# Performance work log

Hardware: AMD Instinct MI355X
Metric: run time of the kernel (lower is better)

Reference implementation:

```python
import jax, jax.numpy as jnp
import numpy as np

B, C, H, W = 8, 512, 64, 64
WS, NH = 8, 16
HD = C // NH
SCALE = float(HD) ** -0.5
L = WS * WS  # tokens per window
BN_EPS = 1e-5


def _rel_index():
    # Swin relative position index, (L, L) int table into (2*WS-1)^2 bias rows
    ch = np.arange(WS)
    coords = np.stack(np.meshgrid(ch, ch, indexing='ij'))  # (2, WS, WS)
    cf = coords.reshape(2, -1)
    rel = cf[:, :, None] - cf[:, None, :]
    rel = rel.transpose(1, 2, 0).copy()
    rel[:, :, 0] += WS - 1
    rel[:, :, 1] += WS - 1
    rel[:, :, 0] *= 2 * WS - 1
    return jnp.asarray(rel.sum(-1))

REL_IDX = _rel_index()


def conv2d(x, w, pad=0, groups=1):
    return jax.lax.conv_general_dilated(
        x, w, (1, 1), [(pad, pad), (pad, pad)],
        feature_group_count=groups,
        dimension_numbers=('NCHW', 'OIHW', 'NCHW'))


def bn(x, g, b):
    # eval-mode BatchNorm with running_mean=0, running_var=1 (fresh init)
    inv = 1.0 / np.sqrt(1.0 + BN_EPS)
    return g[None, :, None, None] * (x * inv) + b[None, :, None, None]


def avgpool(x, kh, kw, ph, pw):
    # torch AvgPool2d: zero padding, count_include_pad=True
    s = jax.lax.reduce_window(x, 0.0, jax.lax.add, (1, 1, kh, kw), (1, 1, 1, 1),
                              ((0, 0), (0, 0), (ph, ph), (pw, pw)))
    return s / (kh * kw)


def setup_inputs() -> dict:
    key = jax.random.key(0)
    ks = jax.random.split(key, 8)
    r = lambda k, s: jax.random.normal(k, s, dtype=jnp.float32) * 0.02
    return {
        'x': jax.random.normal(ks[0], (B, C, H, W), dtype=jnp.float32),
        'w_lc1': r(ks[1], (C, C, 1, 1)),
        'g1': jnp.ones((C,), jnp.float32), 'b1': jnp.zeros((C,), jnp.float32),
        'w_lc2': r(ks[2], (C, C, 3, 3)),
        'g2': jnp.ones((C,), jnp.float32), 'b2': jnp.zeros((C,), jnp.float32),
        'w_qkv': r(ks[3], (3 * C, C, 1, 1)),
        'rel_table': r(ks[4], ((2 * WS - 1) * (2 * WS - 1), NH)),
        'w_dw': r(ks[5], (C, 1, WS, WS)),
        'g3': jnp.ones((C,), jnp.float32), 'b3': jnp.zeros((C,), jnp.float32),
        'w_pw': r(ks[6], (C, C, 1, 1)),
    }


def reference(x, w_lc1, g1, b1, w_lc2, g2, b2, w_qkv, rel_table, w_dw, g3, b3, w_pw):
    # local branch: 1x1 conv+BN  +  3x3 conv+BN
    local = bn(conv2d(x, w_lc1), g1, b1) + bn(conv2d(x, w_lc2, pad=1), g2, b2)

    # H, W divisible by WS -> pad() is a no-op; Hp, Wp = H, W
    hh, ww = H // WS, W // WS
    qkv = conv2d(x, w_qkv)  # (B, 3C, H, W)
    # 'b (qkv h d) (hh ws1) (ww ws2) -> qkv (b hh ww) h (ws1 ws2) d'
    qkv = qkv.reshape(B, 3, NH, HD, hh, WS, ww, WS)
    qkv = qkv.transpose(1, 0, 4, 6, 2, 5, 7, 3).reshape(3, B * hh * ww, NH, L, HD)
    q, k, v = qkv[0], qkv[1], qkv[2]

    dots = jnp.einsum('bhid,bhjd->bhij', q, k) * SCALE  # (Bw, NH, L, L)
    bias = rel_table[REL_IDX]                            # (L, L, NH)
    dots = dots + bias.transpose(2, 0, 1)[None]
    attn = jax.nn.softmax(dots, axis=-1)
    out = jnp.einsum('bhij,bhjd->bhid', attn, v)         # (Bw, NH, L, HD)

    # '(b hh ww) h (ws1 ws2) d -> b (h d) (hh ws1) (ww ws2)'
    out = out.reshape(B, hh, ww, NH, WS, WS, HD)
    out = out.transpose(0, 3, 6, 1, 4, 2, 5).reshape(B, C, H, W)

    ax = avgpool(jnp.pad(out, ((0, 0), (0, 0), (0, 1), (0, 0)), mode='reflect'),
                 WS, 1, WS // 2 - 1, 0)
    ay = avgpool(jnp.pad(out, ((0, 0), (0, 0), (0, 0), (0, 1)), mode='reflect'),
                 1, WS, 0, WS // 2 - 1)
    out = ax + ay + local

    # pad_out + SeparableConvBN(kernel=WS): depthwise conv -> BN -> 1x1 conv
    out = jnp.pad(out, ((0, 0), (0, 0), (0, 1), (0, 1)), mode='reflect')
    out = conv2d(out, w_dw, pad=(WS - 1) // 2, groups=C)
    out = bn(out, g3, b3)
    out = conv2d(out, w_pw)
    return out[:, :, :H, :W]
```

## Files before the change

### kernel.cpp

```cpp
#include <hip/hip_runtime.h>

#define INVBN 0.9999950000374997f
#define ATT_SCALE 0.17677669529663687f

typedef short bf16x8 __attribute__((ext_vector_type(8)));
typedef float f32x4  __attribute__((ext_vector_type(4)));
typedef unsigned short us8v __attribute__((ext_vector_type(8)));

#define AS1C(p) ((const __attribute__((address_space(1))) void*)(p))
#define AS3(p)  ((__attribute__((address_space(3))) void*)(p))

#define VMCNT_BARRIER(Nstr) do {                                   \
    asm volatile("s_waitcnt vmcnt(" Nstr ")" ::: "memory");        \
    __builtin_amdgcn_s_barrier(); } while (0)

__device__ __forceinline__ float bf2f(unsigned short u) {
    return __uint_as_float(((unsigned)u) << 16);
}
__device__ __forceinline__ unsigned short f2bf(float f) {
    unsigned u = __float_as_uint(f);
    u += 0x7FFFu + ((u >> 16) & 1u);
    return (unsigned short)(u >> 16);
}

__global__ __launch_bounds__(256)
void repack_kernel(const float* __restrict__ W2, const float* __restrict__ W1,
                   const float* __restrict__ Wq, const float* __restrict__ Wp,
                   const float* __restrict__ g1, const float* __restrict__ g2,
                   const float* __restrict__ b1, const float* __restrict__ b2,
                   unsigned short* __restrict__ Wt, unsigned short* __restrict__ WqO,
                   unsigned short* __restrict__ WpO, float* __restrict__ bsum)
{
    int i = blockIdx.x * 256 + threadIdx.x;
    if (i < 512) bsum[i] = b1[i] + b2[i];
    if (i < 786432) WqO[i] = f2bf(Wq[i]);
    if (i < 262144) WpO[i] = f2bf(Wp[i]);
    if (i >= 2359296) return;
    int tap = i / 262144;
    int rem = i - tap * 262144;
    int m   = rem >> 9;
    float v = g2[m] * INVBN * W2[(size_t)rem * 9 + tap];
    if (tap == 4) v = fmaf(g1[m] * INVBN, W1[rem], v);
    Wt[i] = f2bf(v);
}

__global__ __launch_bounds__(256)
void bias_precompute_kernel(const float* __restrict__ RT, float* __restrict__ biasM)
{
    int idx = blockIdx.x * 256 + threadIdx.x;
    int h = idx >> 10, rem = idx & 1023;
    int frag = rem >> 6, lane = rem & 63;
    int fi = frag >> 2, fj = frag & 3;
    int q  = 16 * fj + (lane & 15);
    int kb = 16 * fi + ((lane >> 4) << 2);
    int yi = q >> 3, xi = q & 7;
    float4 o;
    float* op = (float*)&o;
#pragma unroll
    for (int r = 0; r < 4; ++r) {
        int j = kb + r;
        int ridx = (yi - (j >> 3) + 7) * 15 + (xi - (j & 7) + 7);
        op[r] = RT[ridx * 16 + h];
    }
    *(float4*)&biasM[(size_t)idx * 4] = o;
}

__global__ __launch_bounds__(256)
void pad_transpose_kernel(const float* __restrict__ X, unsigned short* __restrict__ XT)
{
    int ph = blockIdx.x;
    int b  = blockIdx.y;
    int t  = threadIdx.x;
    unsigned short* rowbase = XT + ((size_t)b * 4356 + (size_t)ph * 66) * 512;
    uint4 z = make_uint4(0, 0, 0, 0);
    if (ph == 0 || ph == 65) {
        uint4* p4 = (uint4*)rowbase;
        for (int i = t; i < 4224; i += 256) p4[i] = z;
        return;
    }
    if (t < 64)       ((uint4*)rowbase)[t] = z;
    else if (t < 128) ((uint4*)(rowbase + 65 * 512))[t - 64] = z;

    int h = ph - 1;
    __shared__ float tile[64][65];
    const float* xb = X + (size_t)b * 512 * 4096 + h * 64;
    for (int cc = 0; cc < 8; ++cc) {
        int c0 = cc * 64;
        __syncthreads();
#pragma unroll
        for (int i = 0; i < 4; ++i) {
            int cl = i * 16 + (t >> 4);
            int w0 = (t & 15) * 4;
            *(float4*)&tile[cl][w0] =
                *(const float4*)&xb[(size_t)(c0 + cl) * 4096 + w0];
        }
        __syncthreads();
#pragma unroll
        for (int it = 0; it < 2; ++it) {
            int wl = it * 32 + (t >> 3);
            int cs = (t & 7) * 8;
            us8v v;
#pragma unroll
            for (int e = 0; e < 8; ++e) v[e] = f2bf(tile[cs + e][wl]);
            *(us8v*)&rowbase[(size_t)(1 + wl) * 512 + c0 + cs] = v;
        }
    }
}

template<int NTAPS>
__global__ __launch_bounds__(512, 2)
void mfma_gemm256(const unsigned short* __restrict__ A,
                  const unsigned short* __restrict__ Bw,
                  const float* __restrict__ bias,
                  unsigned short* __restrict__ Out, int M)
{
    __shared__ __align__(16) unsigned short ldsbuf[65536];

    const int t    = threadIdx.x;
    const int wid  = t >> 6, lane = t & 63;
    const int wr   = wid >> 2, wc = wid & 3;
    const int lrow = lane & 15, lk = lane >> 4;
    const int n0 = blockIdx.x * 256;
    const int m0 = blockIdx.y * 256;
    const int b  = blockIdx.z;
    const unsigned short* Ab = A + (size_t)b * (4356 * 512);
    unsigned short* Ob = Out + (size_t)b * ((size_t)M * 4096);

    const unsigned short* src[4];
    {
        int rsub = lane >> 2, ch = lane & 3;
        int chs  = ch ^ ((rsub >> 1) & 3);
#pragma unroll
        for (int i = 0; i < 4; ++i) {
            if (wid < 4) {
                int p = n0 + (wid * 4 + i) * 16 + rsub;
                int h = p >> 6, w = p & 63;
                src[i] = Ab + (size_t)((h + 1) * 66 + (w + 1)) * 512 + chs * 8;
            } else {
                int m = m0 + ((wid - 4) * 4 + i) * 16 + rsub;
                src[i] = Bw + (size_t)m * 512 + chs * 8;
            }
        }
    }

    f32x4 acc[8][4] = {};

    const int ck0 = (lk ^ ((lrow >> 1) & 3)) * 8;

    auto aScal = [&](int tt) -> int {
        if (NTAPS == 1) return tt * 32;
        int tap = tt >> 4;
        return (tap / 3 - 1) * (66 * 512) + (tap % 3 - 1) * 512 + (tt & 15) * 32;
    };
    auto bScal = [&](int tt) -> int {
        if (NTAPS == 1) return tt * 32;
        return (tt >> 4) * (M * 512) + (tt & 15) * 32;
    };
    auto STAGE = [&](int bufk, int aoff, int boff) {
        int off = (wid < 4) ? aoff : boff;
#pragma unroll
        for (int i = 0; i < 4; ++i)
            __builtin_amdgcn_global_load_lds(
                AS1C(src[i] + off),
                AS3(&ldsbuf[bufk * 16384 + (wid * 4 + i) * 512]), 16, 0, 0);
    };
    auto COMPUTE = [&](int bufk) {
        const unsigned short* Ak = &ldsbuf[bufk * 16384];
        const unsigned short* Bk = &ldsbuf[bufk * 16384 + 8192];
        bf16x8 af[8], bfr[4];
#pragma unroll
        for (int f = 0; f < 8; ++f)
            af[f] = *(const bf16x8*)&Ak[(wr * 128 + f * 16 + lrow) * 32 + ck0];
#pragma unroll
        for (int g = 0; g < 4; ++g)
            bfr[g] = *(const bf16x8*)&Bk[(wc * 64 + g * 16 + lrow) * 32 + ck0];
        __builtin_amdgcn_s_setprio(1);
#pragma unroll
        for (int f = 0; f < 8; ++f)
#pragma unroll
            for (int g = 0; g < 4; ++g)
                acc[f][g] = __builtin_amdgcn_mfma_f32_16x16x32_bf16(
                    af[f], bfr[g], acc[f][g], 0, 0, 0);
        __builtin_amdgcn_s_setprio(0);
    };

    constexpr int NT = NTAPS * 16;

    STAGE(0, aScal(0), bScal(0));
    STAGE(1, aScal(1), bScal(1));
    STAGE(2, aScal(2), bScal(2));
    VMCNT_BARRIER("8");

#pragma unroll 1
    for (int tb = 0; tb < NT - 4; tb += 4) {
        STAGE(3, aScal(tb + 3), bScal(tb + 3)); COMPUTE(0); VMCNT_BARRIER("8");
        STAGE(0, aScal(tb + 4), bScal(tb + 4)); COMPUTE(1); VMCNT_BARRIER("8");
        STAGE(1, aScal(tb + 5), bScal(tb + 5)); COMPUTE(2); VMCNT_BARRIER("8");
        STAGE(2, aScal(tb + 6), bScal(tb + 6)); COMPUTE(3); VMCNT_BARRIER("8");
    }
    STAGE(3, aScal(NT - 1), bScal(NT - 1)); COMPUTE(0); VMCNT_BARRIER("8");
    COMPUTE(1); VMCNT_BARRIER("4");
    COMPUTE(2); VMCNT_BARRIER("0");
    COMPUTE(3);

#pragma unroll
    for (int g = 0; g < 4; ++g) {
        int m = m0 + wc * 64 + g * 16 + lrow;
        float bv = bias ? bias[m] : 0.f;
        size_t mrow = (size_t)m * 4096;
#pragma unroll
        for (int f = 0; f < 8; ++f) {
            int nb = n0 + wr * 128 + f * 16 + lk * 4;
            f32x4 a4 = acc[f][g];
            ushort4 o;
            o.x = f2bf(a4[0] + bv);
            o.y = f2bf(a4[1] + bv);
            o.z = f2bf(a4[2] + bv);
            o.w = f2bf(a4[3] + bv);
            *(ushort4*)&Ob[mrow + nb] = o;
        }
    }
}

__global__ __launch_bounds__(256)
void mfma_gemm_f32out(const unsigned short* __restrict__ A,
                      const unsigned short* __restrict__ Bw,
                      float* __restrict__ Out, int M)
{
    __shared__ short As[128 * 64];
    __shared__ short Bs[128 * 64];

    const int t  = threadIdx.x;
    const int n0 = blockIdx.x * 128;
    const int m0 = blockIdx.y * 128;
    const int b  = blockIdx.z;
    const unsigned short* Ab = A + (size_t)b * (4096 * 512);
    float* Ob = Out + (size_t)b * ((size_t)M * 4096);

    const int trow = t >> 3;
    const int csrc = (t & 7) ^ (trow & 7);
    const unsigned short* aSrc[4];
    const unsigned short* bSrc[4];
#pragma unroll
    for (int i = 0; i < 4; ++i) {
        int r = i * 32 + trow;
        aSrc[i] = Ab + ((size_t)(n0 + r) * 512 + csrc * 8);
        bSrc[i] = Bw + ((size_t)(m0 + r) * 512 + csrc * 8);
    }
    short* aDst = As + (t & 192) * 8;
    short* bDst = Bs + (t & 192) * 8;

    const int lane = t & 63;
    const int wv = t >> 6, wr = wv >> 1, wc = wv & 1;
    const int lrow = lane & 15, lk = lane >> 4;
    int aOff[4][2], bOff[4][2];
#pragma unroll
    for (int f = 0; f < 4; ++f)
#pragma unroll
        for (int kk = 0; kk < 2; ++kk) {
            int ra = wr * 64 + f * 16 + lrow;
            aOff[f][kk] = ra * 64 + ((kk * 4 + lk) ^ (ra & 7)) * 8;
            int rb = wc * 64 + f * 16 + lrow;
            bOff[f][kk] = rb * 64 + ((kk * 4 + lk) ^ (rb & 7)) * 8;
        }

    f32x4 acc[4][4] = {};

#pragma unroll 1
    for (int ks = 0; ks < 8; ++ks) {
        const int k0 = ks * 64;
        __syncthreads();
#pragma unroll
        for (int i = 0; i < 4; ++i) {
            __builtin_amdgcn_global_load_lds(
                AS1C(aSrc[i] + k0), AS3(aDst + i * 2048), 16, 0, 0);
            __builtin_amdgcn_global_load_lds(
                AS1C(bSrc[i] + k0), AS3(bDst + i * 2048), 16, 0, 0);
        }
        __syncthreads();
        bf16x8 av[4][2], bv[4][2];
#pragma unroll
        for (int f = 0; f < 4; ++f) {
            av[f][0] = *(const bf16x8*)&As[aOff[f][0]];
            av[f][1] = *(const bf16x8*)&As[aOff[f][1]];
            bv[f][0] = *(const bf16x8*)&Bs[bOff[f][0]];
            bv[f][1] = *(const bf16x8*)&Bs[bOff[f][1]];
        }
#pragma unroll
        for (int kk = 0; kk < 2; ++kk)
#pragma unroll
            for (int fn = 0; fn < 4; ++fn)
#pragma unroll
                for (int fm = 0; fm < 4; ++fm)
                    acc[fn][fm] = __builtin_amdgcn_mfma_f32_16x16x32_bf16(
                        av[fn][kk], bv[fm][kk], acc[fn][fm], 0, 0, 0);
    }

#pragma unroll
    for (int fm = 0; fm < 4; ++fm) {
        int m = m0 + wc * 64 + fm * 16 + lrow;
        size_t mrow = (size_t)m * 4096;
#pragma unroll
        for (int fn = 0; fn < 4; ++fn) {
            int nb = n0 + wr * 64 + fn * 16 + lk * 4;
            f32x4 a4 = acc[fn][fm];
            *(float4*)&Ob[mrow + nb] = make_float4(a4[0], a4[1], a4[2], a4[3]);
        }
    }
}

__global__ __launch_bounds__(256)
void attn_mfma_kernel(const unsigned short* __restrict__ QKV,
                      const float* __restrict__ biasM,
                      float* __restrict__ OutB)
{
    __shared__ short smem[4 * 9216];
    int t = threadIdx.x;
    int wv = t >> 6, lane = t & 63;
    int wing = blockIdx.x >> 2;
    int head = (blockIdx.x & 3) * 4 + wv;
    int b    = blockIdx.y;
    int hhi = wing >> 3, wwi = wing & 7;
    int sp0 = hhi * 512 + wwi * 8;
    int ch0 = head * 32;
    const unsigned short* Qg = QKV + (size_t)b * 1536 * 4096;

    short* Qtm = smem + wv * 9216;
    short* Ktm = Qtm + 2304;
    short* Pq  = Qtm + 4608;

    {
        int d  = lane & 31;
        int rb = lane >> 5;
#pragma unroll
        for (int i = 0; i < 4; ++i) {
            int r = rb + 2 * i;
            us8v q8 = *(const us8v*)&Qg[(size_t)(ch0 + d) * 4096 + sp0 + r * 64];
            us8v k8 = *(const us8v*)&Qg[(size_t)(512 + ch0 + d) * 4096 + sp0 + r * 64];
#pragma unroll
            for (int e = 0; e < 8; ++e) {
                Qtm[(r * 8 + e) * 36 + d] = (short)q8[e];
                Ktm[(r * 8 + e) * 36 + d] = (short)k8[e];
            }
        }
    }

    int lrow = lane & 15, lk = lane >> 4;

    bf16x8 kf[4], qf[4];
#pragma unroll
    for (int f = 0; f < 4; ++f) {
        kf[f] = *(const bf16x8*)&Ktm[(lrow + 16 * f) * 36 + lk * 8];
        qf[f] = *(const bf16x8*)&Qtm[(lrow + 16 * f) * 36 + lk * 8];
    }
    f32x4 s[4][4] = {};
#pragma unroll
    for (int fi = 0; fi < 4; ++fi)
#pragma unroll
        for (int fj = 0; fj < 4; ++fj)
            s[fi][fj] = __builtin_amdgcn_mfma_f32_16x16x32_bf16(
                kf[fi], qf[fj], s[fi][fj], 0, 0, 0);

    const float* bM = biasM + (size_t)head * 4096;
    float rs[4];
#pragma unroll
    for (int fj = 0; fj < 4; ++fj) {
        float v[4][4];
#pragma unroll
        for (int fi = 0; fi < 4; ++fi) {
            float4 bv = *(const float4*)&bM[((fi * 4 + fj) * 64 + lane) * 4];
            const float* bvp = (const float*)&bv;
#pragma unroll
            for (int r = 0; r < 4; ++r)
                v[fi][r] = fmaf(s[fi][fj][r], ATT_SCALE, bvp[r]);
        }
        float m = -1e30f;
#pragma unroll
        for (int fi = 0; fi < 4; ++fi)
#pragma unroll
            for (int r = 0; r < 4; ++r) m = fmaxf(m, v[fi][r]);
        m = fmaxf(m, __shfl_xor(m, 16));
        m = fmaxf(m, __shfl_xor(m, 32));
        float ev[4][4];
        float sum = 0.f;
#pragma unroll
        for (int fi = 0; fi < 4; ++fi)
#pragma unroll
            for (int r = 0; r < 4; ++r) {
                ev[fi][r] = __expf(v[fi][r] - m);
                sum += ev[fi][r];
            }
        sum += __shfl_xor(sum, 16);
        sum += __shfl_xor(sum, 32);
        rs[fj] = 1.f / sum;
#pragma unroll
        for (int fi = 0; fi < 4; ++fi) {
            unsigned p0 = (unsigned)f2bf(ev[fi][0]) | ((unsigned)f2bf(ev[fi][1]) << 16);
            unsigned p1 = (unsigned)f2bf(ev[fi][2]) | ((unsigned)f2bf(ev[fi][3]) << 16);
            *(uint2*)&Pq[(lrow + 16 * fj) * 72 + 16 * fi + lk * 4] = make_uint2(p0, p1);
        }
    }

    f32x4 o[2][4] = {};
#pragma unroll
    for (int ks = 0; ks < 2; ++ks) {
        bf16x8 vf[2], pf[4];
#pragma unroll
        for (int fid = 0; fid < 2; ++fid)
            vf[fid] = *(const bf16x8*)&Qg[(size_t)(1024 + ch0 + 16 * fid + lrow) * 4096
                                          + sp0 + (lk + 4 * ks) * 64];
#pragma unroll
        for (int fjq = 0; fjq < 4; ++fjq)
            pf[fjq] = *(const bf16x8*)&Pq[(lrow + 16 * fjq) * 72 + ks * 32 + lk * 8];
#pragma unroll
        for (int fid = 0; fid < 2; ++fid)
#pragma unroll
            for (int fjq = 0; fjq < 4; ++fjq)
                o[fid][fjq] = __builtin_amdgcn_mfma_f32_16x16x32_bf16(
                    vf[fid], pf[fjq], o[fid][fjq], 0, 0, 0);
    }

    float* Out = OutB + (size_t)b * 512 * 4096;
#pragma unroll
    for (int fjq = 0; fjq < 4; ++fjq) {
        int q  = lrow + 16 * fjq;
        int sp = sp0 + ((q >> 3) << 6) + (q & 7);
        float rr = rs[fjq];
#pragma unroll
        for (int fid = 0; fid < 2; ++fid)
#pragma unroll
            for (int r = 0; r < 4; ++r) {
                int dch = 16 * fid + lk * 4 + r;
                Out[(size_t)(ch0 + dch) * 4096 + sp] = o[fid][fjq][r] * rr;
            }
    }
}

__global__ __launch_bounds__(256)
void pooldw_kernel(const float* __restrict__ A, const unsigned short* __restrict__ L,
                   const float* __restrict__ Wd,
                   const float* __restrict__ g3, const float* __restrict__ b3,
                   unsigned short* __restrict__ U)
{
    int bc = blockIdx.x;
    int c  = bc & 511;
    __shared__ float pad[72][72];
    int t = threadIdx.x;
    float* pf = &pad[0][0];
#pragma unroll
    for (int i = 0; i < 21; ++i) {
        int e = i * 256 + t;
        if (e < 5184) pf[e] = 0.f;
    }
    __syncthreads();

    const float* ap = A + (size_t)bc * 4096;
#pragma unroll
    for (int i = 0; i < 4; ++i) {
        int idx = i * 256 + t;
        int y = idx >> 4, x4 = (idx & 15) * 4;
        *(float4*)&pad[3 + y][4 + x4] = ((const float4*)ap)[idx];
    }
    if (t < 64)       pad[67][4 + t] = ap[62 * 64 + t];
    else if (t < 128) { int y = t - 64; pad[3 + y][68] = ap[y * 64 + 62]; }
    else if (t == 128) pad[67][68] = ap[62 * 64 + 62];
    __syncthreads();

    const unsigned short* lp = L + (size_t)bc * 4096;
    int u  = t & 15, rr = t >> 4;
    int w0 = u * 4;
    float4 res[4];
#pragma unroll
    for (int g = 0; g < 4; ++g) {
        int h = g * 16 + rr;
        float4 sx = make_float4(0.f, 0.f, 0.f, 0.f);
#pragma unroll
        for (int i = 0; i < 8; ++i) {
            float4 v = *(const float4*)&pad[h + i][4 + w0];
            sx.x += v.x; sx.y += v.y; sx.z += v.z; sx.w += v.w;
        }
        float win[12];
        *(float4*)&win[0] = *(const float4*)&pad[3 + h][w0];
        *(float4*)&win[4] = *(const float4*)&pad[3 + h][w0 + 4];
        *(float4*)&win[8] = *(const float4*)&pad[3 + h][w0 + 8];
        float4 sy = make_float4(0.f, 0.f, 0.f, 0.f);
#pragma unroll
        for (int i = 0; i < 8; ++i) {
            sy.x += win[1 + i];
            sy.y += win[2 + i];
            sy.z += win[3 + i];
            sy.w += win[4 + i];
        }
        ushort4 l4 = *(const ushort4*)&lp[h * 64 + w0];
        res[g].x = fmaf(0.125f, sx.x + sy.x, bf2f(l4.x));
        res[g].y = fmaf(0.125f, sx.y + sy.y, bf2f(l4.y));
        res[g].z = fmaf(0.125f, sx.z + sy.z, bf2f(l4.z));
        res[g].w = fmaf(0.125f, sx.w + sy.w, bf2f(l4.w));
    }
    __syncthreads();

#pragma unroll
    for (int g = 0; g < 4; ++g) {
        int h = g * 16 + rr;
        *(float4*)&pad[3 + h][4 + w0] = res[g];
    }
    __syncthreads();
    if (t < 64)       pad[67][4 + t] = pad[65][4 + t];
    else if (t < 128) { int y = t - 64; pad[3 + y][68] = pad[3 + y][66]; }
    else if (t == 128) pad[67][68] = pad[65][66];
    __syncthreads();

    const float* wdp = Wd + c * 64;
    float gc  = g3[c] * INVBN;
    float bcv = b3[c];
#pragma unroll
    for (int g = 0; g < 4; ++g) {
        int h = g * 16 + rr;
        float a0 = 0.f, a1 = 0.f, a2 = 0.f, a3 = 0.f;
#pragma unroll
        for (int i = 0; i < 8; ++i) {
            float win[12];
            *(float4*)&win[0] = *(const float4*)&pad[h + i][w0];
            *(float4*)&win[4] = *(const float4*)&pad[h + i][w0 + 4];
            *(float4*)&win[8] = *(const float4*)&pad[h + i][w0 + 8];
#pragma unroll
            for (int j = 0; j < 8; ++j) {
                float wv = wdp[i * 8 + j];
                a0 = fmaf(wv, win[1 + j], a0);
                a1 = fmaf(wv, win[2 + j], a1);
                a2 = fmaf(wv, win[3 + j], a2);
                a3 = fmaf(wv, win[4 + j], a3);
            }
        }
        ushort4 o;
        o.x = f2bf(gc * a0 + bcv);
        o.y = f2bf(gc * a1 + bcv);
        o.z = f2bf(gc * a2 + bcv);
        o.w = f2bf(gc * a3 + bcv);
        *(ushort4*)&U[(size_t)bc * 4096 + h * 64 + w0] = o;
    }
}

__global__ __launch_bounds__(256)
void transpose_cp_kernel(const unsigned short* __restrict__ U, unsigned short* __restrict__ Ut)
{
    int pt = blockIdx.x;
    int b  = blockIdx.y;
    const unsigned short* Ub = U + (size_t)b * 512 * 4096;
    unsigned short* Utb = Ut + (size_t)b * 4096 * 512;
    __shared__ unsigned short tile[64][72];
    int t = threadIdx.x;
    int p0 = pt * 64;

    for (int cc = 0; cc < 8; ++cc) {
        int c0 = cc * 64;
        __syncthreads();
        {
            int cl = t >> 2, px = (t & 3) * 16;
            const unsigned short* src = &Ub[(size_t)(c0 + cl) * 4096 + p0 + px];
            *(us8v*)&tile[cl][px]     = *(const us8v*)src;
            *(us8v*)&tile[cl][px + 8] = *(const us8v*)(src + 8);
        }
        __syncthreads();
        {
            int pl = t >> 2, cx = (t & 3) * 16;
            us8v o0, o1;
#pragma unroll
            for (int e = 0; e < 8; ++e) {
                o0[e] = tile[cx + e][pl];
                o1[e] = tile[cx + 8 + e][pl];
            }
            unsigned short* dst = &Utb[(size_t)(p0 + pl) * 512 + c0 + cx];
            *(us8v*)dst       = o0;
            *(us8v*)(dst + 8) = o1;
        }
    }
}

extern "C" void kernel_launch(void* const* d_in, const int* in_sizes, int n_in,
                              void* d_out, int out_size, void* d_ws, size_t ws_size,
                              hipStream_t stream)
{
    (void)in_sizes; (void)n_in; (void)out_size;
    const float* x     = (const float*)d_in[0];
    const float* w_lc1 = (const float*)d_in[1];
    const float* g1    = (const float*)d_in[2];
    const float* b1    = (const float*)d_in[3];
    const float* w_lc2 = (const float*)d_in[4];
    const float* g2    = (const float*)d_in[5];
    const float* b2    = (const float*)d_in[6];
    const float* w_qkv = (const float*)d_in[7];
    const float* rt    = (const float*)d_in[8];
    const float* w_dw  = (const float*)d_in[9];
    const float* g3    = (const float*)d_in[10];
    const float* b3    = (const float*)d_in[11];
    const float* w_pw  = (const float*)d_in[12];
    float* out = (float*)d_out;

    unsigned short* S        = (unsigned short*)d_ws;
    unsigned short* local_us = S;
    unsigned short* xt_us    = S + 16777216;
    unsigned short* u_us     = xt_us;
    unsigned short* wt3_us   = S + 34619392;
    unsigned short* wq_us    = S + 36978688;
    unsigned short* wpw_us   = S + 37765120;
    float*          bsum     = (float*)(S + 38027264);
    float*          biasM    = (float*)(S + 38028288);
    unsigned short* qkv_us   = S + 38552576;
    unsigned short* ut_us    = local_us;

    const bool full = ws_size >= (size_t)(38552576 + 50331648) * 2;

    repack_kernel<<<dim3(9216), 256, 0, stream>>>(w_lc2, w_lc1, w_qkv, w_pw,
                                                  g1, g2, b1, b2,
                                                  wt3_us, wq_us, wpw_us, bsum);
    bias_precompute_kernel<<<dim3(64), 256, 0, stream>>>(rt, biasM);
    pad_transpose_kernel<<<dim3(66, 8), 256, 0, stream>>>(x, xt_us);
    mfma_gemm256<9><<<dim3(16, 2, 8), 512, 0, stream>>>(
        xt_us, wt3_us, bsum, local_us, 512);

    if (full) {
        mfma_gemm256<1><<<dim3(16, 6, 8), 512, 0, stream>>>(
            xt_us, wq_us, nullptr, qkv_us, 1536);
        attn_mfma_kernel<<<dim3(256, 8), 256, 0, stream>>>(qkv_us, biasM, out);
    } else {
        for (int b = 0; b < 8; ++b) {
            mfma_gemm256<1><<<dim3(16, 6, 1), 512, 0, stream>>>(
                xt_us + (size_t)b * 4356 * 512, wq_us, nullptr, qkv_us, 1536);
            attn_mfma_kernel<<<dim3(256, 1), 256, 0, stream>>>(
                qkv_us, biasM, out + (size_t)b * 2097152);
        }
    }

    pooldw_kernel<<<dim3(4096), 256, 0, stream>>>(out, local_us, w_dw, g3, b3, u_us);
    transpose_cp_kernel<<<dim3(64, 8), 256, 0, stream>>>(u_us, ut_us);
    mfma_gemm_f32out<<<dim3(32, 4, 8), 256, 0, stream>>>(
        ut_us, wpw_us, out, 512);
}
```

Before: 473.9 us.

## Split GEMM k-step into interleaved halves and store attention output as bf16

The 256x256 MFMA GEMM main loop is restructured so each k-tile runs as two half-steps. Each half issues half of the next stage's global-to-LDS loads, with barriers between the LDS fragment reads and the MFMA bursts, so loads, LDS traffic and matrix math overlap more finely. Separately, the attention kernel now writes its output as bf16 into a workspace buffer aliased with the input-transpose region instead of fp32 into the final output, and the pool/depthwise kernel reads bf16. This halves the attention write and read traffic, at the cost of extra barriers per tile and reduced precision of the intermediate.

```diff
diff --git a/kernel.cpp b/kernel.cpp
--- a/kernel.cpp
+++ b/kernel.cpp
@@ -9,10 +9,6 @@
 
 #define AS1C(p) ((const __attribute__((address_space(1))) void*)(p))
 #define AS3(p)  ((__attribute__((address_space(3))) void*)(p))
-
-#define VMCNT_BARRIER(Nstr) do {                                   \
-    asm volatile("s_waitcnt vmcnt(" Nstr ")" ::: "memory");        \
-    __builtin_amdgcn_s_barrier(); } while (0)
 
 __device__ __forceinline__ float bf2f(unsigned short u) {
     return __uint_as_float(((unsigned)u) << 16);
@@ -107,6 +103,41 @@
     }
 }
 
+#define MF(A,B,C) __builtin_amdgcn_mfma_f32_16x16x32_bf16((A),(B),(C),0,0,0)
+
+#define TILE(BUF, SBUF, SAO, SBO, DOSTAGE, DOVM, VMSTR) do {                  \
+    bf16x8 aa[4], bb[4];                                                      \
+    _Pragma("unroll")                                                         \
+    for (int f = 0; f < 4; ++f) {                                             \
+        aa[f] = *(const bf16x8*)&ldsbuf[(BUF)*16384 + (wr*128 + f*16 + lrow)*32 + ck0]; \
+        bb[f] = *(const bf16x8*)&ldsbuf[(BUF)*16384 + 8192 + (wc*64 + f*16 + lrow)*32 + ck0]; \
+    }                                                                         \
+    if (DOSTAGE) STAGEH((SBUF), (SAO), (SBO), 0);                             \
+    __builtin_amdgcn_s_barrier();                                             \
+    __builtin_amdgcn_s_setprio(1);                                            \
+    _Pragma("unroll")                                                         \
+    for (int f = 0; f < 4; ++f)                                               \
+        _Pragma("unroll")                                                     \
+        for (int g = 0; g < 4; ++g)                                           \
+            acc[f][g] = MF(aa[f], bb[g], acc[f][g]);                          \
+    __builtin_amdgcn_s_setprio(0);                                            \
+    __builtin_amdgcn_s_barrier();                                             \
+    _Pragma("unroll")                                                         \
+    for (int f = 0; f < 4; ++f)                                               \
+        aa[f] = *(const bf16x8*)&ldsbuf[(BUF)*16384 + (wr*128 + (f+4)*16 + lrow)*32 + ck0]; \
+    if (DOSTAGE) STAGEH((SBUF), (SAO), (SBO), 1);                             \
+    if (DOVM) { asm volatile("s_waitcnt vmcnt(" VMSTR ")" ::: "memory"); }    \
+    __builtin_amdgcn_s_barrier();                                             \
+    __builtin_amdgcn_s_setprio(1);                                            \
+    _Pragma("unroll")                                                         \
+    for (int f = 0; f < 4; ++f)                                               \
+        _Pragma("unroll")                                                     \
+        for (int g = 0; g < 4; ++g)                                           \
+            acc[f+4][g] = MF(aa[f], bb[g], acc[f+4][g]);                      \
+    __builtin_amdgcn_s_setprio(0);                                            \
+    __builtin_amdgcn_s_barrier();                                             \
+} while (0)
+
 template<int NTAPS>
 __global__ __launch_bounds__(512, 2)
 void mfma_gemm256(const unsigned short* __restrict__ A,
@@ -144,7 +175,6 @@
     }
 
     f32x4 acc[8][4] = {};
-
     const int ck0 = (lk ^ ((lrow >> 1) & 3)) * 8;
 
     auto aScal = [&](int tt) -> int {
@@ -156,52 +186,34 @@
         if (NTAPS == 1) return tt * 32;
         return (tt >> 4) * (M * 512) + (tt & 15) * 32;
     };
-    auto STAGE = [&](int bufk, int aoff, int boff) {
+    auto STAGEH = [&](int bufk, int aoff, int boff, int half) {
         int off = (wid < 4) ? aoff : boff;
 #pragma unroll
-        for (int i = 0; i < 4; ++i)
+        for (int i = 2 * half; i < 2 * half + 2; ++i)
             __builtin_amdgcn_global_load_lds(
                 AS1C(src[i] + off),
                 AS3(&ldsbuf[bufk * 16384 + (wid * 4 + i) * 512]), 16, 0, 0);
     };
-    auto COMPUTE = [&](int bufk) {
-        const unsigned short* Ak = &ldsbuf[bufk * 16384];
-        const unsigned short* Bk = &ldsbuf[bufk * 16384 + 8192];
-        bf16x8 af[8], bfr[4];
-#pragma unroll
-        for (int f = 0; f < 8; ++f)
-            af[f] = *(const bf16x8*)&Ak[(wr * 128 + f * 16 + lrow) * 32 + ck0];
-#pragma unroll
-        for (int g = 0; g < 4; ++g)
-            bfr[g] = *(const bf16x8*)&Bk[(wc * 64 + g * 16 + lrow) * 32 + ck0];
-        __builtin_amdgcn_s_setprio(1);
-#pragma unroll
-        for (int f = 0; f < 8; ++f)
-#pragma unroll
-            for (int g = 0; g < 4; ++g)
-                acc[f][g] = __builtin_amdgcn_mfma_f32_16x16x32_bf16(
-                    af[f], bfr[g], acc[f][g], 0, 0, 0);
-        __builtin_amdgcn_s_setprio(0);
-    };
 
     constexpr int NT = NTAPS * 16;
 
-    STAGE(0, aScal(0), bScal(0));
-    STAGE(1, aScal(1), bScal(1));
-    STAGE(2, aScal(2), bScal(2));
-    VMCNT_BARRIER("8");
+    STAGEH(0, aScal(0), bScal(0), 0); STAGEH(0, aScal(0), bScal(0), 1);
+    STAGEH(1, aScal(1), bScal(1), 0); STAGEH(1, aScal(1), bScal(1), 1);
+    STAGEH(2, aScal(2), bScal(2), 0); STAGEH(2, aScal(2), bScal(2), 1);
+    asm volatile("s_waitcnt vmcnt(8)" ::: "memory");
+    __builtin_amdgcn_s_barrier();
 
 #pragma unroll 1
     for (int tb = 0; tb < NT - 4; tb += 4) {
-        STAGE(3, aScal(tb + 3), bScal(tb + 3)); COMPUTE(0); VMCNT_BARRIER("8");
-        STAGE(0, aScal(tb + 4), bScal(tb + 4)); COMPUTE(1); VMCNT_BARRIER("8");
-        STAGE(1, aScal(tb + 5), bScal(tb + 5)); COMPUTE(2); VMCNT_BARRIER("8");
-        STAGE(2, aScal(tb + 6), bScal(tb + 6)); COMPUTE(3); VMCNT_BARRIER("8");
-    }
-    STAGE(3, aScal(NT - 1), bScal(NT - 1)); COMPUTE(0); VMCNT_BARRIER("8");
-    COMPUTE(1); VMCNT_BARRIER("4");
-    COMPUTE(2); VMCNT_BARRIER("0");
-    COMPUTE(3);
+        TILE(0, 3, aScal(tb + 3), bScal(tb + 3), 1, 1, "8");
+        TILE(1, 0, aScal(tb + 4), bScal(tb + 4), 1, 1, "8");
+        TILE(2, 1, aScal(tb + 5), bScal(tb + 5), 1, 1, "8");
+        TILE(3, 2, aScal(tb + 6), bScal(tb + 6), 1, 1, "8");
+    }
+    TILE(0, 3, aScal(NT - 1), bScal(NT - 1), 1, 1, "8");
+    TILE(1, 0, 0, 0, 0, 1, "4");
+    TILE(2, 0, 0, 0, 0, 1, "0");
+    TILE(3, 0, 0, 0, 0, 0, "0");
 
 #pragma unroll
     for (int g = 0; g < 4; ++g) {
@@ -312,7 +324,7 @@
 __global__ __launch_bounds__(256)
 void attn_mfma_kernel(const unsigned short* __restrict__ QKV,
                       const float* __restrict__ biasM,
-                      float* __restrict__ OutB)
+                      unsigned short* __restrict__ OutB)
 {
     __shared__ short smem[4 * 9216];
     int t = threadIdx.x;
@@ -420,7 +432,7 @@
                     vf[fid], pf[fjq], o[fid][fjq], 0, 0, 0);
     }
 
-    float* Out = OutB + (size_t)b * 512 * 4096;
+    unsigned short* Out = OutB + (size_t)b * 512 * 4096;
 #pragma unroll
     for (int fjq = 0; fjq < 4; ++fjq) {
         int q  = lrow + 16 * fjq;
@@ -431,13 +443,13 @@
 #pragma unroll
             for (int r = 0; r < 4; ++r) {
                 int dch = 16 * fid + lk * 4 + r;
-                Out[(size_t)(ch0 + dch) * 4096 + sp] = o[fid][fjq][r] * rr;
+                Out[(size_t)(ch0 + dch) * 4096 + sp] = f2bf(o[fid][fjq][r] * rr);
             }
     }
 }
 
 __global__ __launch_bounds__(256)
-void pooldw_kernel(const float* __restrict__ A, const unsigned short* __restrict__ L,
+void pooldw_kernel(const unsigned short* __restrict__ A, const unsigned short* __restrict__ L,
                    const float* __restrict__ Wd,
                    const float* __restrict__ g3, const float* __restrict__ b3,
                    unsigned short* __restrict__ U)
@@ -454,16 +466,18 @@
     }
     __syncthreads();
 
-    const float* ap = A + (size_t)bc * 4096;
+    const unsigned short* ap = A + (size_t)bc * 4096;
 #pragma unroll
     for (int i = 0; i < 4; ++i) {
         int idx = i * 256 + t;
         int y = idx >> 4, x4 = (idx & 15) * 4;
-        *(float4*)&pad[3 + y][4 + x4] = ((const float4*)ap)[idx];
-    }
-    if (t < 64)       pad[67][4 + t] = ap[62 * 64 + t];
-    else if (t < 128) { int y = t - 64; pad[3 + y][68] = ap[y * 64 + 62]; }
-    else if (t == 128) pad[67][68] = ap[62 * 64 + 62];
+        ushort4 a4 = ((const ushort4*)ap)[idx];
+        *(float4*)&pad[3 + y][4 + x4] =
+            make_float4(bf2f(a4.x), bf2f(a4.y), bf2f(a4.z), bf2f(a4.w));
+    }
+    if (t < 64)       pad[67][4 + t] = bf2f(ap[62 * 64 + t]);
+    else if (t < 128) { int y = t - 64; pad[3 + y][68] = bf2f(ap[y * 64 + 62]); }
+    else if (t == 128) pad[67][68] = bf2f(ap[62 * 64 + 62]);
     __syncthreads();
 
     const unsigned short* lp = L + (size_t)bc * 4096;
@@ -600,6 +614,7 @@
     unsigned short* S        = (unsigned short*)d_ws;
     unsigned short* local_us = S;
     unsigned short* xt_us    = S + 16777216;
+    unsigned short* attnO    = xt_us;
     unsigned short* u_us     = xt_us;
     unsigned short* wt3_us   = S + 34619392;
     unsigned short* wq_us    = S + 36978688;
@@ -622,17 +637,17 @@
     if (full) {
         mfma_gemm256<1><<<dim3(16, 6, 8), 512, 0, stream>>>(
             xt_us, wq_us, nullptr, qkv_us, 1536);
-        attn_mfma_kernel<<<dim3(256, 8), 256, 0, stream>>>(qkv_us, biasM, out);
+        attn_mfma_kernel<<<dim3(256, 8), 256, 0, stream>>>(qkv_us, biasM, attnO);
     } else {
         for (int b = 0; b < 8; ++b) {
             mfma_gemm256<1><<<dim3(16, 6, 1), 512, 0, stream>>>(
                 xt_us + (size_t)b * 4356 * 512, wq_us, nullptr, qkv_us, 1536);
             attn_mfma_kernel<<<dim3(256, 1), 256, 0, stream>>>(
-                qkv_us, biasM, out + (size_t)b * 2097152);
-        }
-    }
-
-    pooldw_kernel<<<dim3(4096), 256, 0, stream>>>(out, local_us, w_dw, g3, b3, u_us);
+                qkv_us, biasM, attnO + (size_t)b * 2097152);
+        }
+    }
+
+    pooldw_kernel<<<dim3(4096), 256, 0, stream>>>(attnO, local_us, w_dw, g3, b3, u_us);
     transpose_cp_kernel<<<dim3(64, 8), 256, 0, stream>>>(u_us, ut_us);
     mfma_gemm_f32out<<<dim3(32, 4, 8), 256, 0, stream>>>(
         ut_us, wpw_us, out, 512);
```

Result: no change. 465.8 us (-1.7%).

## Shrink GEMM tiles to 256x128 with double buffering, XCD-swizzled grid, bf16 attention output

Applied to the files above, without the earlier changes.

The bf16 GEMM now runs 256-thread blocks on 256x128 tiles. Its 4-stage LDS ring becomes a smaller 2-stage double buffer, and a 1D grid is remapped so that consecutive tiles land on the same XCD. The attention output is written as bf16 into workspace instead of fp32 into the output buffer, and the pooling kernel reads and converts it. The goal is higher occupancy, better L2 locality and less attention write/read traffic. The cost is shallower prefetch with two barriers per k-step, and extra bf16 rounding of the attention output.

```diff
diff --git a/kernel.cpp b/kernel.cpp
--- a/kernel.cpp
+++ b/kernel.cpp
@@ -9,10 +9,6 @@
 
 #define AS1C(p) ((const __attribute__((address_space(1))) void*)(p))
 #define AS3(p)  ((__attribute__((address_space(3))) void*)(p))
-
-#define VMCNT_BARRIER(Nstr) do {                                   \
-    asm volatile("s_waitcnt vmcnt(" Nstr ")" ::: "memory");        \
-    __builtin_amdgcn_s_barrier(); } while (0)
 
 __device__ __forceinline__ float bf2f(unsigned short u) {
     return __uint_as_float(((unsigned)u) << 16);
@@ -108,43 +104,47 @@
 }
 
 template<int NTAPS>
-__global__ __launch_bounds__(512, 2)
+__global__ __launch_bounds__(256, 2)
 void mfma_gemm256(const unsigned short* __restrict__ A,
                   const unsigned short* __restrict__ Bw,
                   const float* __restrict__ bias,
-                  unsigned short* __restrict__ Out, int M)
-{
-    __shared__ __align__(16) unsigned short ldsbuf[65536];
+                  unsigned short* __restrict__ Out, int M, int MB)
+{
+    __shared__ __align__(16) unsigned short ldsbuf[24576];
 
     const int t    = threadIdx.x;
     const int wid  = t >> 6, lane = t & 63;
-    const int wr   = wid >> 2, wc = wid & 3;
+    const int wr   = wid >> 1, wc = wid & 1;
     const int lrow = lane & 15, lk = lane >> 4;
-    const int n0 = blockIdx.x * 256;
-    const int m0 = blockIdx.y * 256;
-    const int b  = blockIdx.z;
-    const unsigned short* Ab = A + (size_t)b * (4356 * 512);
-    unsigned short* Ob = Out + (size_t)b * ((size_t)M * 4096);
-
-    const unsigned short* src[4];
-    {
-        int rsub = lane >> 2, ch = lane & 3;
-        int chs  = ch ^ ((rsub >> 1) & 3);
-#pragma unroll
-        for (int i = 0; i < 4; ++i) {
-            if (wid < 4) {
-                int p = n0 + (wid * 4 + i) * 16 + rsub;
-                int h = p >> 6, w = p & 63;
-                src[i] = Ab + (size_t)((h + 1) * 66 + (w + 1)) * 512 + chs * 8;
-            } else {
-                int m = m0 + ((wid - 4) * 4 + i) * 16 + rsub;
-                src[i] = Bw + (size_t)m * 512 + chs * 8;
-            }
-        }
-    }
+
+    const int nwg = gridDim.x;
+    const int id  = blockIdx.x;
+    const int cid = (id & 7) * (nwg >> 3) + (id >> 3);
+    const int by  = cid % MB;
+    const int rst = cid / MB;
+    const int bx  = rst & 15;
+    const int bz  = rst >> 4;
+
+    const int n0 = bx * 256;
+    const int m0 = by * 128;
+    const unsigned short* Ab = A + (size_t)bz * (4356 * 512);
+    unsigned short* Ob = Out + (size_t)bz * ((size_t)M * 4096);
+
+    const int rsub = t >> 2, ch = t & 3;
+    const int chs  = ch ^ ((rsub >> 1) & 3);
+    const unsigned short* asrc[4];
+    const unsigned short* bsrc[2];
+#pragma unroll
+    for (int i = 0; i < 4; ++i) {
+        int p = n0 + i * 64 + rsub;
+        int h = p >> 6, w = p & 63;
+        asrc[i] = Ab + (size_t)((h + 1) * 66 + (w + 1)) * 512 + chs * 8;
+    }
+#pragma unroll
+    for (int j = 0; j < 2; ++j)
+        bsrc[j] = Bw + (size_t)(m0 + j * 64 + rsub) * 512 + chs * 8;
 
     f32x4 acc[8][4] = {};
-
     const int ck0 = (lk ^ ((lrow >> 1) & 3)) * 8;
 
     auto aScal = [&](int tt) -> int {
@@ -156,52 +156,53 @@
         if (NTAPS == 1) return tt * 32;
         return (tt >> 4) * (M * 512) + (tt & 15) * 32;
     };
-    auto STAGE = [&](int bufk, int aoff, int boff) {
-        int off = (wid < 4) ? aoff : boff;
+    auto STAGE = [&](int parity, int tt) {
+        unsigned short* dst = ldsbuf + parity * 12288;
+        int ao = aScal(tt), bo = bScal(tt);
 #pragma unroll
         for (int i = 0; i < 4; ++i)
             __builtin_amdgcn_global_load_lds(
-                AS1C(src[i] + off),
-                AS3(&ldsbuf[bufk * 16384 + (wid * 4 + i) * 512]), 16, 0, 0);
+                AS1C(asrc[i] + ao), AS3(dst + (i * 64 + rsub) * 32 + ch * 8), 16, 0, 0);
+#pragma unroll
+        for (int j = 0; j < 2; ++j)
+            __builtin_amdgcn_global_load_lds(
+                AS1C(bsrc[j] + bo), AS3(dst + 8192 + (j * 64 + rsub) * 32 + ch * 8), 16, 0, 0);
     };
-    auto COMPUTE = [&](int bufk) {
-        const unsigned short* Ak = &ldsbuf[bufk * 16384];
-        const unsigned short* Bk = &ldsbuf[bufk * 16384 + 8192];
-        bf16x8 af[8], bfr[4];
+    auto COMPUTE = [&](int parity) {
+        const unsigned short* Ak = ldsbuf + parity * 12288;
+        const unsigned short* Bk = Ak + 8192;
+        bf16x8 af[8], bf[4];
 #pragma unroll
         for (int f = 0; f < 8; ++f)
             af[f] = *(const bf16x8*)&Ak[(wr * 128 + f * 16 + lrow) * 32 + ck0];
 #pragma unroll
         for (int g = 0; g < 4; ++g)
-            bfr[g] = *(const bf16x8*)&Bk[(wc * 64 + g * 16 + lrow) * 32 + ck0];
+            bf[g] = *(const bf16x8*)&Bk[(wc * 64 + g * 16 + lrow) * 32 + ck0];
         __builtin_amdgcn_s_setprio(1);
 #pragma unroll
         for (int f = 0; f < 8; ++f)
 #pragma unroll
             for (int g = 0; g < 4; ++g)
                 acc[f][g] = __builtin_amdgcn_mfma_f32_16x16x32_bf16(
-                    af[f], bfr[g], acc[f][g], 0, 0, 0);
+                    af[f], bf[g], acc[f][g], 0, 0, 0);
         __builtin_amdgcn_s_setprio(0);
     };
 
     constexpr int NT = NTAPS * 16;
 
-    STAGE(0, aScal(0), bScal(0));
-    STAGE(1, aScal(1), bScal(1));
-    STAGE(2, aScal(2), bScal(2));
-    VMCNT_BARRIER("8");
-
-#pragma unroll 1
-    for (int tb = 0; tb < NT - 4; tb += 4) {
-        STAGE(3, aScal(tb + 3), bScal(tb + 3)); COMPUTE(0); VMCNT_BARRIER("8");
-        STAGE(0, aScal(tb + 4), bScal(tb + 4)); COMPUTE(1); VMCNT_BARRIER("8");
-        STAGE(1, aScal(tb + 5), bScal(tb + 5)); COMPUTE(2); VMCNT_BARRIER("8");
-        STAGE(2, aScal(tb + 6), bScal(tb + 6)); COMPUTE(3); VMCNT_BARRIER("8");
-    }
-    STAGE(3, aScal(NT - 1), bScal(NT - 1)); COMPUTE(0); VMCNT_BARRIER("8");
-    COMPUTE(1); VMCNT_BARRIER("4");
-    COMPUTE(2); VMCNT_BARRIER("0");
-    COMPUTE(3);
+    STAGE(0, 0);
+#pragma unroll 2
+    for (int tt = 0; tt < NT; ++tt) {
+        if (tt + 1 < NT) {
+            STAGE((tt + 1) & 1, tt + 1);
+            asm volatile("s_waitcnt vmcnt(6)" ::: "memory");
+        } else {
+            asm volatile("s_waitcnt vmcnt(0)" ::: "memory");
+        }
+        __builtin_amdgcn_s_barrier();
+        COMPUTE(tt & 1);
+        __builtin_amdgcn_s_barrier();
+    }
 
 #pragma unroll
     for (int g = 0; g < 4; ++g) {
@@ -312,7 +313,7 @@
 __global__ __launch_bounds__(256)
 void attn_mfma_kernel(const unsigned short* __restrict__ QKV,
                       const float* __restrict__ biasM,
-                      float* __restrict__ OutB)
+                      unsigned short* __restrict__ OutB)
 {
     __shared__ short smem[4 * 9216];
     int t = threadIdx.x;
@@ -420,7 +421,7 @@
                     vf[fid], pf[fjq], o[fid][fjq], 0, 0, 0);
     }
 
-    float* Out = OutB + (size_t)b * 512 * 4096;
+    unsigned short* Out = OutB + (size_t)b * 512 * 4096;
 #pragma unroll
     for (int fjq = 0; fjq < 4; ++fjq) {
         int q  = lrow + 16 * fjq;
@@ -431,13 +432,13 @@
 #pragma unroll
             for (int r = 0; r < 4; ++r) {
                 int dch = 16 * fid + lk * 4 + r;
-                Out[(size_t)(ch0 + dch) * 4096 + sp] = o[fid][fjq][r] * rr;
+                Out[(size_t)(ch0 + dch) * 4096 + sp] = f2bf(o[fid][fjq][r] * rr);
             }
     }
 }
 
 __global__ __launch_bounds__(256)
-void pooldw_kernel(const float* __restrict__ A, const unsigned short* __restrict__ L,
+void pooldw_kernel(const unsigned short* __restrict__ A, const unsigned short* __restrict__ L,
                    const float* __restrict__ Wd,
                    const float* __restrict__ g3, const float* __restrict__ b3,
                    unsigned short* __restrict__ U)
@@ -454,16 +455,18 @@
     }
     __syncthreads();
 
-    const float* ap = A + (size_t)bc * 4096;
+    const unsigned short* ap = A + (size_t)bc * 4096;
 #pragma unroll
     for (int i = 0; i < 4; ++i) {
         int idx = i * 256 + t;
         int y = idx >> 4, x4 = (idx & 15) * 4;
-        *(float4*)&pad[3 + y][4 + x4] = ((const float4*)ap)[idx];
-    }
-    if (t < 64)       pad[67][4 + t] = ap[62 * 64 + t];
-    else if (t < 128) { int y = t - 64; pad[3 + y][68] = ap[y * 64 + 62]; }
-    else if (t == 128) pad[67][68] = ap[62 * 64 + 62];
+        ushort4 a4 = ((const ushort4*)ap)[idx];
+        *(float4*)&pad[3 + y][4 + x4] =
+            make_float4(bf2f(a4.x), bf2f(a4.y), bf2f(a4.z), bf2f(a4.w));
+    }
+    if (t < 64)       pad[67][4 + t] = bf2f(ap[62 * 64 + t]);
+    else if (t < 128) { int y = t - 64; pad[3 + y][68] = bf2f(ap[y * 64 + 62]); }
+    else if (t == 128) pad[67][68] = bf2f(ap[62 * 64 + 62]);
     __syncthreads();
 
     const unsigned short* lp = L + (size_t)bc * 4096;
@@ -600,6 +603,7 @@
     unsigned short* S        = (unsigned short*)d_ws;
     unsigned short* local_us = S;
     unsigned short* xt_us    = S + 16777216;
+    unsigned short* attnO    = xt_us;
     unsigned short* u_us     = xt_us;
     unsigned short* wt3_us   = S + 34619392;
     unsigned short* wq_us    = S + 36978688;
@@ -616,23 +620,23 @@
                                                   wt3_us, wq_us, wpw_us, bsum);
     bias_precompute_kernel<<<dim3(64), 256, 0, stream>>>(rt, biasM);
     pad_transpose_kernel<<<dim3(66, 8), 256, 0, stream>>>(x, xt_us);
-    mfma_gemm256<9><<<dim3(16, 2, 8), 512, 0, stream>>>(
-        xt_us, wt3_us, bsum, local_us, 512);
+    mfma_gemm256<9><<<dim3(512), 256, 0, stream>>>(
+        xt_us, wt3_us, bsum, local_us, 512, 4);
 
     if (full) {
-        mfma_gemm256<1><<<dim3(16, 6, 8), 512, 0, stream>>>(
-            xt_us, wq_us, nullptr, qkv_us, 1536);
-        attn_mfma_kernel<<<dim3(256, 8), 256, 0, stream>>>(qkv_us, biasM, out);
+        mfma_gemm256<1><<<dim3(1536), 256, 0, stream>>>(
+            xt_us, wq_us, nullptr, qkv_us, 1536, 12);
+        attn_mfma_kernel<<<dim3(256, 8), 256, 0, stream>>>(qkv_us, biasM, attnO);
     } else {
         for (int b = 0; b < 8; ++b) {
-            mfma_gemm256<1><<<dim3(16, 6, 1), 512, 0, stream>>>(
-                xt_us + (size_t)b * 4356 * 512, wq_us, nullptr, qkv_us, 1536);
+            mfma_gemm256<1><<<dim3(192), 256, 0, stream>>>(
+                xt_us + (size_t)b * 4356 * 512, wq_us, nullptr, qkv_us, 1536, 12);
             attn_mfma_kernel<<<dim3(256, 1), 256, 0, stream>>>(
-                qkv_us, biasM, out + (size_t)b * 2097152);
-        }
-    }
-
-    pooldw_kernel<<<dim3(4096), 256, 0, stream>>>(out, local_us, w_dw, g3, b3, u_us);
+                qkv_us, biasM, attnO + (size_t)b * 2097152);
+        }
+    }
+
+    pooldw_kernel<<<dim3(4096), 256, 0, stream>>>(attnO, local_us, w_dw, g3, b3, u_us);
     transpose_cp_kernel<<<dim3(64, 8), 256, 0, stream>>>(u_us, ut_us);
     mfma_gemm_f32out<<<dim3(32, 4, 8), 256, 0, stream>>>(
         ut_us, wpw_us, out, 512);
```

New measurement: 481.2 us. Within noise of the previous version (+1.6%).
